# Kernel optimization log

Hardware: AMD Instinct MI355X
Metric: run time of the kernel (lower is better)

Reference implementation:

```python
import jax, jax.numpy as jnp
import numpy as np

ENC_DIM, DEC_DIM, ATT_DIM = 2048, 512, 512

def setup_inputs() -> dict:
    key = jax.random.key(0)
    ks = jax.random.split(key, 8)
    s_enc = 1.0 / np.sqrt(ENC_DIM)
    s_dec = 1.0 / np.sqrt(DEC_DIM)
    s_att = 1.0 / np.sqrt(ATT_DIM)
    return {
        "encoder_out": jax.random.normal(ks[0], (256, 196, ENC_DIM), jnp.float32),
        "decoder_hidden": jax.random.normal(ks[1], (256, DEC_DIM), jnp.float32),
        "W_enc": jax.random.uniform(ks[2], (ENC_DIM, ATT_DIM), jnp.float32, -s_enc, s_enc),
        "b_enc": jax.random.uniform(ks[3], (ATT_DIM,), jnp.float32, -s_enc, s_enc),
        "W_dec": jax.random.uniform(ks[4], (DEC_DIM, ATT_DIM), jnp.float32, -s_dec, s_dec),
        "b_dec": jax.random.uniform(ks[5], (ATT_DIM,), jnp.float32, -s_dec, s_dec),
        "W_att": jax.random.uniform(ks[6], (ATT_DIM, 1), jnp.float32, -s_att, s_att),
        "b_att": jax.random.uniform(ks[7], (1,), jnp.float32, -s_att, s_att),
    }

def reference(encoder_out, decoder_hidden, W_enc, b_enc, W_dec, b_dec, W_att, b_att):
    # att1: (B, P, A); att2: (B, 1, A)
    att1 = jnp.einsum('bpe,ea->bpa', encoder_out, W_enc) + b_enc
    att2 = (decoder_hidden @ W_dec + b_dec)[:, None, :]
    # scalar score per pixel: (B, P)
    e = (jax.nn.relu(att1 + att2) @ W_att)[..., 0] + b_att[0]
    alpha = jax.nn.softmax(e, axis=-1)  # softmax over pixels
    z = jnp.einsum('bpe,bp->be', encoder_out, alpha)
    return (z, alpha)
```

## Files before the change

kernel.cpp:

```cpp
#include <hip/hip_runtime.h>
#include <hip/hip_bf16.h>

#define ENC_DIM 2048
#define DEC_DIM 512
#define ATT_DIM 512
#define NB 256
#define NP 196
#define M_TOT (NB * NP)
#define BM 64
#define BK 32
#define NSTEP (ENC_DIM / BK)

typedef __attribute__((ext_vector_type(8))) short short8;
typedef __attribute__((ext_vector_type(4))) short short4s;
typedef __attribute__((ext_vector_type(4))) float f32x4;

__device__ __forceinline__ short4s cvt4(f32x4 v) {
    union { short4s s; __hip_bfloat16 h[4]; } u;
    u.h[0] = __float2bfloat16(v[0]);
    u.h[1] = __float2bfloat16(v[1]);
    u.h[2] = __float2bfloat16(v[2]);
    u.h[3] = __float2bfloat16(v[3]);
    return u.s;
}

__global__ __launch_bounds__(256) void prep_kernel(const float* __restrict__ W,
                                                   __hip_bfloat16* __restrict__ Btt,
                                                   const float* __restrict__ dec,
                                                   const float* __restrict__ W_dec,
                                                   const float* __restrict__ b_dec,
                                                   const float* __restrict__ b_enc,
                                                   float* __restrict__ att2f) {
    __shared__ float ds[DEC_DIM];
    if (blockIdx.x < 512) {
        const int gid = blockIdx.x * 256 + threadIdx.x;
        const int s   = gid >> 11;
        const int u   = gid & 2047;
        const int fr  = u >> 6;
        const int kg  = (u >> 4) & 3;
        const int l15 = u & 15;
        const int col = fr * 16 + l15;
        const int k0  = s * 32 + kg * 8;
        union { short8 v; __hip_bfloat16 h[8]; } x;
        #pragma unroll
        for (int i = 0; i < 8; ++i)
            x.h[i] = __float2bfloat16(W[(size_t)(k0 + i) * ATT_DIM + col]);
        *(short8*)((short*)Btt + (size_t)gid * 8) = x.v;
    } else {
        const int b = blockIdx.x - 512;
        const int t = threadIdx.x;
        ds[t]       = dec[(size_t)b * DEC_DIM + t];
        ds[t + 256] = dec[(size_t)b * DEC_DIM + t + 256];
        __syncthreads();
        #pragma unroll
        for (int j = 0; j < 2; ++j) {
            const int n = t + j * 256;
            float s = 0.f;
            #pragma unroll 8
            for (int k = 0; k < DEC_DIM; ++k)
                s += ds[k] * W_dec[(size_t)k * ATT_DIM + n];
            att2f[(size_t)b * ATT_DIM + n] = s + b_dec[n] + b_enc[n];
        }
    }
}

__global__ __launch_bounds__(512, 2) void e_kernel(const float* __restrict__ enc,
                                                   const short* __restrict__ Btt,
                                                   const float* __restrict__ att2f,
                                                   const float* __restrict__ W_att,
                                                   float* __restrict__ e_out) {
    __shared__ __attribute__((aligned(16))) short As[2][2048];
    __shared__ float ebuf[8][64];

    const int tid  = threadIdx.x;
    const int lane = tid & 63;
    const int wv   = tid >> 6;
    const int l15  = lane & 15;
    const int kg   = lane >> 4;
    const int M0   = blockIdx.x * BM;

    const int arow = tid >> 3;
    const int aq   = tid & 7;
    const float* asrc = enc + (size_t)(M0 + arow) * ENC_DIM + aq * 4;
    const int awr = (arow >> 4) * 512 + (aq >> 1) * 128 + (arow & 15) * 8 + (aq & 1) * 4;

    const short* pBb = Btt + wv * 2048 + kg * 128 + l15 * 8;

    f32x4 acc[4][4];
    #pragma unroll
    for (int i = 0; i < 4; ++i)
        #pragma unroll
        for (int j = 0; j < 4; ++j)
            acc[i][j] = (f32x4){0.f, 0.f, 0.f, 0.f};

#define MFMA16(A0, A1, A2, A3, B0, B1, B2, B3)                                              \
    acc[0][0] = __builtin_amdgcn_mfma_f32_16x16x32_bf16(A0, B0, acc[0][0], 0, 0, 0);        \
    acc[0][1] = __builtin_amdgcn_mfma_f32_16x16x32_bf16(A0, B1, acc[0][1], 0, 0, 0);        \
    acc[0][2] = __builtin_amdgcn_mfma_f32_16x16x32_bf16(A0, B2, acc[0][2], 0, 0, 0);        \
    acc[0][3] = __builtin_amdgcn_mfma_f32_16x16x32_bf16(A0, B3, acc[0][3], 0, 0, 0);        \
    acc[1][0] = __builtin_amdgcn_mfma_f32_16x16x32_bf16(A1, B0, acc[1][0], 0, 0, 0);        \
    acc[1][1] = __builtin_amdgcn_mfma_f32_16x16x32_bf16(A1, B1, acc[1][1], 0, 0, 0);        \
    acc[1][2] = __builtin_amdgcn_mfma_f32_16x16x32_bf16(A1, B2, acc[1][2], 0, 0, 0);        \
    acc[1][3] = __builtin_amdgcn_mfma_f32_16x16x32_bf16(A1, B3, acc[1][3], 0, 0, 0);        \
    acc[2][0] = __builtin_amdgcn_mfma_f32_16x16x32_bf16(A2, B0, acc[2][0], 0, 0, 0);        \
    acc[2][1] = __builtin_amdgcn_mfma_f32_16x16x32_bf16(A2, B1, acc[2][1], 0, 0, 0);        \
    acc[2][2] = __builtin_amdgcn_mfma_f32_16x16x32_bf16(A2, B2, acc[2][2], 0, 0, 0);        \
    acc[2][3] = __builtin_amdgcn_mfma_f32_16x16x32_bf16(A2, B3, acc[2][3], 0, 0, 0);        \
    acc[3][0] = __builtin_amdgcn_mfma_f32_16x16x32_bf16(A3, B0, acc[3][0], 0, 0, 0);        \
    acc[3][1] = __builtin_amdgcn_mfma_f32_16x16x32_bf16(A3, B1, acc[3][1], 0, 0, 0);        \
    acc[3][2] = __builtin_amdgcn_mfma_f32_16x16x32_bf16(A3, B2, acc[3][2], 0, 0, 0);        \
    acc[3][3] = __builtin_amdgcn_mfma_f32_16x16x32_bf16(A3, B3, acc[3][3], 0, 0, 0);

    *(short4s*)&As[0][awr] = cvt4(*(const f32x4*)asrc);
    short8 c0 = *(const short8*)(pBb);
    short8 c1 = *(const short8*)(pBb + 512);
    short8 c2 = *(const short8*)(pBb + 1024);
    short8 c3 = *(const short8*)(pBb + 1536);
    f32x4 avP = *(const f32x4*)(asrc + BK);
    asm volatile("s_waitcnt lgkmcnt(0)" ::: "memory");
    __builtin_amdgcn_s_barrier();
    __builtin_amdgcn_sched_barrier(0);

    for (int s = 0; s < NSTEP; s += 2) {
        const short* p1 = pBb + (size_t)((s + 1) & 63) * 16384;
        short8 n0 = *(const short8*)(p1);
        short8 n1 = *(const short8*)(p1 + 512);
        short8 n2 = *(const short8*)(p1 + 1024);
        short8 n3 = *(const short8*)(p1 + 1536);
        f32x4 avN0 = *(const f32x4*)(asrc + (size_t)((s + 2) & 63) * BK);
        __builtin_amdgcn_sched_barrier(0);
        {
            const short* Ac = &As[0][0];
            const short8 a0 = *(const short8*)&Ac[0 * 512 + lane * 8];
            const short8 a1 = *(const short8*)&Ac[1 * 512 + lane * 8];
            const short8 a2 = *(const short8*)&Ac[2 * 512 + lane * 8];
            const short8 a3 = *(const short8*)&Ac[3 * 512 + lane * 8];
            __builtin_amdgcn_s_setprio(1);
            MFMA16(a0, a1, a2, a3, c0, c1, c2, c3)
            __builtin_amdgcn_s_setprio(0);
        }
        *(short4s*)&As[1][awr] = cvt4(avP);
        avP = avN0;
        asm volatile("s_waitcnt lgkmcnt(0)" ::: "memory");
        __builtin_amdgcn_s_barrier();
        __builtin_amdgcn_sched_barrier(0);

        const short* p2 = pBb + (size_t)((s + 2) & 63) * 16384;
        c0 = *(const short8*)(p2);
        c1 = *(const short8*)(p2 + 512);
        c2 = *(const short8*)(p2 + 1024);
        c3 = *(const short8*)(p2 + 1536);
        f32x4 avN1 = *(const f32x4*)(asrc + (size_t)((s + 3) & 63) * BK);
        __builtin_amdgcn_sched_barrier(0);
        {
            const short* Ac = &As[1][0];
            const short8 a0 = *(const short8*)&Ac[0 * 512 + lane * 8];
            const short8 a1 = *(const short8*)&Ac[1 * 512 + lane * 8];
            const short8 a2 = *(const short8*)&Ac[2 * 512 + lane * 8];
            const short8 a3 = *(const short8*)&Ac[3 * 512 + lane * 8];
            __builtin_amdgcn_s_setprio(1);
            MFMA16(a0, a1, a2, a3, n0, n1, n2, n3)
            __builtin_amdgcn_s_setprio(0);
        }
        *(short4s*)&As[0][awr] = cvt4(avP);
        avP = avN1;
        asm volatile("s_waitcnt lgkmcnt(0)" ::: "memory");
        __builtin_amdgcn_s_barrier();
        __builtin_amdgcn_sched_barrier(0);
    }
#undef MFMA16

    float wat[4];
    #pragma unroll
    for (int nf = 0; nf < 4; ++nf) wat[nf] = W_att[wv * 64 + nf * 16 + l15];

    #pragma unroll
    for (int mf = 0; mf < 4; ++mf) {
        #pragma unroll
        for (int rr = 0; rr < 4; ++rr) {
            const int ml = mf * 16 + kg * 4 + rr;
            const int bb = (M0 + ml) / NP;
            const float* arow2 = att2f + (size_t)bb * ATT_DIM + wv * 64 + l15;
            float sv = 0.f;
            #pragma unroll
            for (int nf = 0; nf < 4; ++nf) {
                float v = acc[mf][nf][rr] + arow2[nf * 16];
                sv += fmaxf(v, 0.f) * wat[nf];
            }
            sv += __shfl_xor(sv, 1);
            sv += __shfl_xor(sv, 2);
            sv += __shfl_xor(sv, 4);
            sv += __shfl_xor(sv, 8);
            if (l15 == 0) ebuf[wv][ml] = sv;
        }
    }
    __syncthreads();
    if (tid < 64) {
        float sv = 0.f;
        #pragma unroll
        for (int w = 0; w < 8; ++w) sv += ebuf[w][tid];
        e_out[M0 + tid] = sv;
    }
}

__global__ __launch_bounds__(256) void z_kernel(const float* __restrict__ enc,
                                                const float* __restrict__ e,
                                                float* __restrict__ z,
                                                float* __restrict__ alpha) {
    const int b  = blockIdx.x;
    const int cb = blockIdx.y;
    const int t  = threadIdx.x;
    __shared__ float al[NP];
    __shared__ float red[4];

    float ev = (t < NP) ? e[(size_t)b * NP + t] : -1e30f;
    float m = ev;
    #pragma unroll
    for (int o = 32; o > 0; o >>= 1) m = fmaxf(m, __shfl_xor(m, o));
    if ((t & 63) == 0) red[t >> 6] = m;
    __syncthreads();
    m = fmaxf(fmaxf(red[0], red[1]), fmaxf(red[2], red[3]));
    __syncthreads();
    float ex = (t < NP) ? __expf(ev - m) : 0.f;
    float s = ex;
    #pragma unroll
    for (int o = 32; o > 0; o >>= 1) s += __shfl_xor(s, o);
    if ((t & 63) == 0) red[t >> 6] = s;
    __syncthreads();
    s = red[0] + red[1] + red[2] + red[3];
    const float a = ex * (1.0f / s);
    if (t < NP) {
        al[t] = a;
        if (cb == 0) alpha[(size_t)b * NP + t] = a;
    }
    __syncthreads();

    const int c0 = cb * 1024 + t * 4;
    const float4* ep = (const float4*)(enc + (size_t)b * NP * ENC_DIM + c0);
    float4 z0 = make_float4(0.f, 0.f, 0.f, 0.f);
    float4 z1 = make_float4(0.f, 0.f, 0.f, 0.f);
    #pragma unroll 4
    for (int p = 0; p < NP; p += 2) {
        const float a0 = al[p];
        const float a1 = al[p + 1];
        const float4 v0 = ep[(size_t)p * (ENC_DIM / 4)];
        const float4 v1 = ep[(size_t)(p + 1) * (ENC_DIM / 4)];
        z0.x += a0 * v0.x; z0.y += a0 * v0.y; z0.z += a0 * v0.z; z0.w += a0 * v0.w;
        z1.x += a1 * v1.x; z1.y += a1 * v1.y; z1.z += a1 * v1.z; z1.w += a1 * v1.w;
    }
    z0.x += z1.x; z0.y += z1.y; z0.z += z1.z; z0.w += z1.w;
    *(float4*)(z + (size_t)b * ENC_DIM + c0) = z0;
}

extern "C" void kernel_launch(void* const* d_in, const int* in_sizes, int n_in,
                              void* d_out, int out_size, void* d_ws, size_t ws_size,
                              hipStream_t stream) {
    const float* enc   = (const float*)d_in[0];
    const float* dec   = (const float*)d_in[1];
    const float* W_enc = (const float*)d_in[2];
    const float* b_enc = (const float*)d_in[3];
    const float* W_dec = (const float*)d_in[4];
    const float* b_dec = (const float*)d_in[5];
    const float* W_att = (const float*)d_in[6];

    float* z     = (float*)d_out;
    float* alpha = z + (size_t)NB * ENC_DIM;

    char* ws = (char*)d_ws;
    __hip_bfloat16* Btt = (__hip_bfloat16*)ws;
    float* att2f        = (float*)(ws + 2 * 1024 * 1024);
    float* e            = (float*)(ws + 2 * 1024 * 1024 + 512 * 1024);

    prep_kernel<<<768, 256, 0, stream>>>(W_enc, Btt, dec, W_dec, b_dec, b_enc, att2f);
    e_kernel<<<M_TOT / BM, 512, 0, stream>>>(enc, (const short*)Btt, att2f, W_att, e);
    z_kernel<<<dim3(NB, 2), 256, 0, stream>>>(enc, e, z, alpha);
}
```

Before: 301.4 us.

## Load A operand directly from global into registers, dropping LDS staging and barriers

Each wave now reads its own fp32 encoder rows straight from global memory in the MFMA fragment layout and converts them to bf16 in registers, instead of staging a shared bf16 tile in LDS with a barrier per k-step. The B fragment loads become nontemporal. This removes the LDS round trip and the block-wide synchronisation. In exchange, every one of the 8 waves re-reads the same 64x32 A slice, so global/L2 traffic for A rises roughly eightfold, and the extra in-flight registers may hurt occupancy.

```diff
diff --git a/kernel.cpp b/kernel.cpp
--- a/kernel.cpp
+++ b/kernel.cpp
@@ -12,16 +12,19 @@
 #define NSTEP (ENC_DIM / BK)
 
 typedef __attribute__((ext_vector_type(8))) short short8;
-typedef __attribute__((ext_vector_type(4))) short short4s;
 typedef __attribute__((ext_vector_type(4))) float f32x4;
 
-__device__ __forceinline__ short4s cvt4(f32x4 v) {
-    union { short4s s; __hip_bfloat16 h[4]; } u;
-    u.h[0] = __float2bfloat16(v[0]);
-    u.h[1] = __float2bfloat16(v[1]);
-    u.h[2] = __float2bfloat16(v[2]);
-    u.h[3] = __float2bfloat16(v[3]);
-    return u.s;
+__device__ __forceinline__ short8 cvt8v(f32x4 x, f32x4 y) {
+    union { short8 v; __hip_bfloat16 h[8]; } u;
+    u.h[0] = __float2bfloat16(x[0]);
+    u.h[1] = __float2bfloat16(x[1]);
+    u.h[2] = __float2bfloat16(x[2]);
+    u.h[3] = __float2bfloat16(x[3]);
+    u.h[4] = __float2bfloat16(y[0]);
+    u.h[5] = __float2bfloat16(y[1]);
+    u.h[6] = __float2bfloat16(y[2]);
+    u.h[7] = __float2bfloat16(y[3]);
+    return u.v;
 }
 
 __global__ __launch_bounds__(256) void prep_kernel(const float* __restrict__ W,
@@ -69,7 +72,6 @@
                                                    const float* __restrict__ att2f,
                                                    const float* __restrict__ W_att,
                                                    float* __restrict__ e_out) {
-    __shared__ __attribute__((aligned(16))) short As[2][2048];
     __shared__ float ebuf[8][64];
 
     const int tid  = threadIdx.x;
@@ -79,11 +81,7 @@
     const int kg   = lane >> 4;
     const int M0   = blockIdx.x * BM;
 
-    const int arow = tid >> 3;
-    const int aq   = tid & 7;
-    const float* asrc = enc + (size_t)(M0 + arow) * ENC_DIM + aq * 4;
-    const int awr = (arow >> 4) * 512 + (aq >> 1) * 128 + (arow & 15) * 8 + (aq & 1) * 4;
-
+    const float* asA = enc + (size_t)(M0 + l15) * ENC_DIM + kg * 8;
     const short* pBb = Btt + wv * 2048 + kg * 128 + l15 * 8;
 
     f32x4 acc[4][4];
@@ -93,82 +91,77 @@
         for (int j = 0; j < 4; ++j)
             acc[i][j] = (f32x4){0.f, 0.f, 0.f, 0.f};
 
-#define MFMA16(A0, A1, A2, A3, B0, B1, B2, B3)                                              \
-    acc[0][0] = __builtin_amdgcn_mfma_f32_16x16x32_bf16(A0, B0, acc[0][0], 0, 0, 0);        \
-    acc[0][1] = __builtin_amdgcn_mfma_f32_16x16x32_bf16(A0, B1, acc[0][1], 0, 0, 0);        \
-    acc[0][2] = __builtin_amdgcn_mfma_f32_16x16x32_bf16(A0, B2, acc[0][2], 0, 0, 0);        \
-    acc[0][3] = __builtin_amdgcn_mfma_f32_16x16x32_bf16(A0, B3, acc[0][3], 0, 0, 0);        \
-    acc[1][0] = __builtin_amdgcn_mfma_f32_16x16x32_bf16(A1, B0, acc[1][0], 0, 0, 0);        \
-    acc[1][1] = __builtin_amdgcn_mfma_f32_16x16x32_bf16(A1, B1, acc[1][1], 0, 0, 0);        \
-    acc[1][2] = __builtin_amdgcn_mfma_f32_16x16x32_bf16(A1, B2, acc[1][2], 0, 0, 0);        \
-    acc[1][3] = __builtin_amdgcn_mfma_f32_16x16x32_bf16(A1, B3, acc[1][3], 0, 0, 0);        \
-    acc[2][0] = __builtin_amdgcn_mfma_f32_16x16x32_bf16(A2, B0, acc[2][0], 0, 0, 0);        \
-    acc[2][1] = __builtin_amdgcn_mfma_f32_16x16x32_bf16(A2, B1, acc[2][1], 0, 0, 0);        \
-    acc[2][2] = __builtin_amdgcn_mfma_f32_16x16x32_bf16(A2, B2, acc[2][2], 0, 0, 0);        \
-    acc[2][3] = __builtin_amdgcn_mfma_f32_16x16x32_bf16(A2, B3, acc[2][3], 0, 0, 0);        \
-    acc[3][0] = __builtin_amdgcn_mfma_f32_16x16x32_bf16(A3, B0, acc[3][0], 0, 0, 0);        \
-    acc[3][1] = __builtin_amdgcn_mfma_f32_16x16x32_bf16(A3, B1, acc[3][1], 0, 0, 0);        \
-    acc[3][2] = __builtin_amdgcn_mfma_f32_16x16x32_bf16(A3, B2, acc[3][2], 0, 0, 0);        \
+    short8 c0, c1, c2, c3, n0, n1, n2, n3;
+    f32x4 x00, x01, x10, x11, x20, x21, x30, x31;
+    f32x4 y00, y01, y10, y11, y20, y21, y30, y31;
+
+#define LOADB(d0, d1, d2, d3, S)                                        \
+    {                                                                   \
+        const short* p = pBb + (size_t)(S) * 16384;                     \
+        d0 = __builtin_nontemporal_load((const short8*)(p));            \
+        d1 = __builtin_nontemporal_load((const short8*)(p + 512));      \
+        d2 = __builtin_nontemporal_load((const short8*)(p + 1024));     \
+        d3 = __builtin_nontemporal_load((const short8*)(p + 1536));     \
+    }
+#define LOADA(d00, d01, d10, d11, d20, d21, d30, d31, S)                \
+    {                                                                   \
+        const float* p = asA + (size_t)(S) * 32;                        \
+        d00 = *(const f32x4*)(p);          d01 = *(const f32x4*)(p + 4);            \
+        d10 = *(const f32x4*)(p + 32768);  d11 = *(const f32x4*)(p + 32768 + 4);    \
+        d20 = *(const f32x4*)(p + 65536);  d21 = *(const f32x4*)(p + 65536 + 4);    \
+        d30 = *(const f32x4*)(p + 98304);  d31 = *(const f32x4*)(p + 98304 + 4);    \
+    }
+#define MFMA16(A0, A1, A2, A3, B0, B1, B2, B3)                                       \
+    acc[0][0] = __builtin_amdgcn_mfma_f32_16x16x32_bf16(A0, B0, acc[0][0], 0, 0, 0); \
+    acc[0][1] = __builtin_amdgcn_mfma_f32_16x16x32_bf16(A0, B1, acc[0][1], 0, 0, 0); \
+    acc[0][2] = __builtin_amdgcn_mfma_f32_16x16x32_bf16(A0, B2, acc[0][2], 0, 0, 0); \
+    acc[0][3] = __builtin_amdgcn_mfma_f32_16x16x32_bf16(A0, B3, acc[0][3], 0, 0, 0); \
+    acc[1][0] = __builtin_amdgcn_mfma_f32_16x16x32_bf16(A1, B0, acc[1][0], 0, 0, 0); \
+    acc[1][1] = __builtin_amdgcn_mfma_f32_16x16x32_bf16(A1, B1, acc[1][1], 0, 0, 0); \
+    acc[1][2] = __builtin_amdgcn_mfma_f32_16x16x32_bf16(A1, B2, acc[1][2], 0, 0, 0); \
+    acc[1][3] = __builtin_amdgcn_mfma_f32_16x16x32_bf16(A1, B3, acc[1][3], 0, 0, 0); \
+    acc[2][0] = __builtin_amdgcn_mfma_f32_16x16x32_bf16(A2, B0, acc[2][0], 0, 0, 0); \
+    acc[2][1] = __builtin_amdgcn_mfma_f32_16x16x32_bf16(A2, B1, acc[2][1], 0, 0, 0); \
+    acc[2][2] = __builtin_amdgcn_mfma_f32_16x16x32_bf16(A2, B2, acc[2][2], 0, 0, 0); \
+    acc[2][3] = __builtin_amdgcn_mfma_f32_16x16x32_bf16(A2, B3, acc[2][3], 0, 0, 0); \
+    acc[3][0] = __builtin_amdgcn_mfma_f32_16x16x32_bf16(A3, B0, acc[3][0], 0, 0, 0); \
+    acc[3][1] = __builtin_amdgcn_mfma_f32_16x16x32_bf16(A3, B1, acc[3][1], 0, 0, 0); \
+    acc[3][2] = __builtin_amdgcn_mfma_f32_16x16x32_bf16(A3, B2, acc[3][2], 0, 0, 0); \
     acc[3][3] = __builtin_amdgcn_mfma_f32_16x16x32_bf16(A3, B3, acc[3][3], 0, 0, 0);
 
-    *(short4s*)&As[0][awr] = cvt4(*(const f32x4*)asrc);
-    short8 c0 = *(const short8*)(pBb);
-    short8 c1 = *(const short8*)(pBb + 512);
-    short8 c2 = *(const short8*)(pBb + 1024);
-    short8 c3 = *(const short8*)(pBb + 1536);
-    f32x4 avP = *(const f32x4*)(asrc + BK);
-    asm volatile("s_waitcnt lgkmcnt(0)" ::: "memory");
-    __builtin_amdgcn_s_barrier();
-    __builtin_amdgcn_sched_barrier(0);
+    LOADB(c0, c1, c2, c3, 0)
+    LOADA(x00, x01, x10, x11, x20, x21, x30, x31, 0)
+    LOADB(n0, n1, n2, n3, 1)
+    LOADA(y00, y01, y10, y11, y20, y21, y30, y31, 1)
 
     for (int s = 0; s < NSTEP; s += 2) {
-        const short* p1 = pBb + (size_t)((s + 1) & 63) * 16384;
-        short8 n0 = *(const short8*)(p1);
-        short8 n1 = *(const short8*)(p1 + 512);
-        short8 n2 = *(const short8*)(p1 + 1024);
-        short8 n3 = *(const short8*)(p1 + 1536);
-        f32x4 avN0 = *(const f32x4*)(asrc + (size_t)((s + 2) & 63) * BK);
-        __builtin_amdgcn_sched_barrier(0);
         {
-            const short* Ac = &As[0][0];
-            const short8 a0 = *(const short8*)&Ac[0 * 512 + lane * 8];
-            const short8 a1 = *(const short8*)&Ac[1 * 512 + lane * 8];
-            const short8 a2 = *(const short8*)&Ac[2 * 512 + lane * 8];
-            const short8 a3 = *(const short8*)&Ac[3 * 512 + lane * 8];
+            const short8 a0 = cvt8v(x00, x01);
+            const short8 a1 = cvt8v(x10, x11);
+            const short8 a2 = cvt8v(x20, x21);
+            const short8 a3 = cvt8v(x30, x31);
             __builtin_amdgcn_s_setprio(1);
             MFMA16(a0, a1, a2, a3, c0, c1, c2, c3)
             __builtin_amdgcn_s_setprio(0);
         }
-        *(short4s*)&As[1][awr] = cvt4(avP);
-        avP = avN0;
-        asm volatile("s_waitcnt lgkmcnt(0)" ::: "memory");
-        __builtin_amdgcn_s_barrier();
-        __builtin_amdgcn_sched_barrier(0);
-
-        const short* p2 = pBb + (size_t)((s + 2) & 63) * 16384;
-        c0 = *(const short8*)(p2);
-        c1 = *(const short8*)(p2 + 512);
-        c2 = *(const short8*)(p2 + 1024);
-        c3 = *(const short8*)(p2 + 1536);
-        f32x4 avN1 = *(const f32x4*)(asrc + (size_t)((s + 3) & 63) * BK);
-        __builtin_amdgcn_sched_barrier(0);
+        LOADB(c0, c1, c2, c3, (s + 2) & 63)
+        LOADA(x00, x01, x10, x11, x20, x21, x30, x31, (s + 2) & 63)
+
         {
-            const short* Ac = &As[1][0];
-            const short8 a0 = *(const short8*)&Ac[0 * 512 + lane * 8];
-            const short8 a1 = *(const short8*)&Ac[1 * 512 + lane * 8];
-            const short8 a2 = *(const short8*)&Ac[2 * 512 + lane * 8];
-            const short8 a3 = *(const short8*)&Ac[3 * 512 + lane * 8];
+            const short8 a0 = cvt8v(y00, y01);
+            const short8 a1 = cvt8v(y10, y11);
+            const short8 a2 = cvt8v(y20, y21);
+            const short8 a3 = cvt8v(y30, y31);
             __builtin_amdgcn_s_setprio(1);
             MFMA16(a0, a1, a2, a3, n0, n1, n2, n3)
             __builtin_amdgcn_s_setprio(0);
         }
-        *(short4s*)&As[0][awr] = cvt4(avP);
-        avP = avN1;
-        asm volatile("s_waitcnt lgkmcnt(0)" ::: "memory");
-        __builtin_amdgcn_s_barrier();
-        __builtin_amdgcn_sched_barrier(0);
+        LOADB(n0, n1, n2, n3, (s + 3) & 63)
+        LOADA(y00, y01, y10, y11, y20, y21, y30, y31, (s + 3) & 63)
     }
 #undef MFMA16
+#undef LOADA
+#undef LOADB
 
     float wat[4];
     #pragma unroll
```

Result: slower. 689.0 us (+128.6%).
